# Optimization experiments

Measured on AMD Instinct MI355X. Metric: run time of the kernel, lower is better.

The kernel has to match this reference:

```python
import jax, jax.numpy as jnp
import numpy as np

S, B, D = 2048, 4, 1024

def setup_inputs() -> dict:
    key = jax.random.key(0)
    ks = jax.random.split(key, 7)
    std = 1.0 / np.sqrt(D)
    return {
        "x": jax.random.normal(ks[0], (S, B, D), dtype=jnp.float32),
        "Wq": jax.random.normal(ks[1], (D, D), dtype=jnp.float32) * std,
        "bq": jax.random.normal(ks[2], (D,), dtype=jnp.float32) * std,
        "Wk": jax.random.normal(ks[3], (D, D), dtype=jnp.float32) * std,
        "bk": jax.random.normal(ks[4], (D,), dtype=jnp.float32) * std,
        "Wv": jax.random.normal(ks[5], (D, D), dtype=jnp.float32) * std,
        "bv": jax.random.normal(ks[6], (D,), dtype=jnp.float32) * std,
    }

def reference(x, Wq, bq, Wk, bk, Wv, bv):
    # x: (S, B, D); flatten(start_dim=2) is a no-op for 3D input
    xf = jnp.transpose(x, (1, 0, 2))  # (B, S, D)
    # torch Linear: y = x @ W.T + b (W is (out, in))
    q = jnp.einsum('bsd,ed->bse', xf, Wq) + bq
    k = jnp.einsum('bsd,ed->bse', xf, Wk) + bk
    v = jnp.einsum('bsd,ed->bse', xf, Wv) + bv
    scale = 1.0 / jnp.sqrt(jnp.asarray(x.shape[-1], dtype=x.dtype))
    scores = jnp.einsum('bqd,bkd->bqk', q, k) * scale  # (B, S, S)
    attn = jax.nn.softmax(scores, axis=-1)
    weighted = jnp.einsum('bqk,bkd->bqd', attn, v)  # (B, S, D)
    # Faithful to torch.reshape(weighted, x.shape): reshape, NOT transpose back
    return jnp.reshape(weighted, x.shape)
```

## Files before the change

kernel.cpp:

```cpp
#include <hip/hip_runtime.h>
#include <math.h>

typedef float  f4   __attribute__((ext_vector_type(4)));
typedef float  f32x4 __attribute__((ext_vector_type(4)));
typedef short  bf16x8 __attribute__((ext_vector_type(8)));
typedef unsigned short u16x8 __attribute__((ext_vector_type(8)));

#define S_ 2048
#define B_ 4
#define D_ 1024

__device__ __forceinline__ unsigned short f2bf(float f) {
    unsigned u = __builtin_bit_cast(unsigned, f);
    u = (u + 0x7FFFu + ((u >> 16) & 1u)) >> 16;
    return (unsigned short)u;
}

#define GLOAD16(gsrc, ldst) \
    __builtin_amdgcn_global_load_lds((const __attribute__((address_space(1))) void*)(gsrc), \
                                     (__attribute__((address_space(3))) void*)(ldst), 16, 0, 0)


__global__ __launch_bounds__(128)
void convert_x(const float* __restrict__ x, unsigned short* __restrict__ xb)
{
    const int bid = blockIdx.x;
    const int b = bid & (B_ - 1);
    const int s = bid >> 2;
    const int t = threadIdx.x;
    const float* in = x + (size_t)bid * D_ + t * 8;
    unsigned short* out = xb + ((size_t)b * S_ + s) * D_ + t * 8;
    f4 lo = *(const f4*)in;
    f4 hi = *(const f4*)(in + 4);
    u16x8 o;
#pragma unroll
    for (int j = 0; j < 4; j++) { o[j] = f2bf(lo[j]); o[4 + j] = f2bf(hi[j]); }
    *(u16x8*)out = o;
}

__global__ __launch_bounds__(256)
void convert_w(const float* __restrict__ W0, const float* __restrict__ W1,
               const float* __restrict__ W2, unsigned short* __restrict__ dst)
{
    const float* src = (blockIdx.z == 0) ? W0 : (blockIdx.z == 1) ? W1 : W2;
    unsigned short* d = dst + (size_t)blockIdx.z * D_ * D_;
    size_t i = ((size_t)blockIdx.x * 256 + threadIdx.x) * 8;
    f4 lo = *(const f4*)(src + i);
    f4 hi = *(const f4*)(src + i + 4);
    u16x8 o;
#pragma unroll
    for (int j = 0; j < 4; j++) { o[j] = f2bf(lo[j]); o[4 + j] = f2bf(hi[j]); }
    *(u16x8*)(d + i) = o;
}

__global__ __launch_bounds__(256)
void transpose_v(const unsigned short* __restrict__ vb, unsigned short* __restrict__ vt)
{
    __shared__ unsigned short tile[64][66];
    const int t = threadIdx.x;
    const int s0 = blockIdx.x * 64, d0 = blockIdx.y * 64, b = blockIdx.z;
    const int rr = t >> 3, c8 = (t & 7) * 8;
#pragma unroll
    for (int p = 0; p < 2; p++) {
        int r = rr + p * 32;
        u16x8 v = *(const u16x8*)(vb + ((size_t)b * S_ + s0 + r) * D_ + d0 + c8);
#pragma unroll
        for (int j = 0; j < 8; j++) tile[r][c8 + j] = v[j];
    }
    __syncthreads();
#pragma unroll
    for (int p = 0; p < 2; p++) {
        int r = rr + p * 32;
        u16x8 o;
#pragma unroll
        for (int j = 0; j < 8; j++) o[j] = tile[c8 + j][r];
        *(u16x8*)(vt + ((size_t)b * D_ + d0 + r) * S_ + s0 + c8) = o;
    }
}

template<bool BIAS, bool OBF16>
__global__ __launch_bounds__(256)
void gemm_bt(const unsigned short* __restrict__ A, const unsigned short* __restrict__ B,
             const float* __restrict__ bias, void* __restrict__ C,
             int lda, int ldb, int ldc, int K, float alpha,
             size_t sA, size_t sB, size_t sC)
{
    __shared__ unsigned short sm[8192];

    const unsigned short* Ab = A + blockIdx.z * sA;
    const unsigned short* Bb = B + blockIdx.z * sB;

    const int t   = threadIdx.x;
    const int w   = t >> 6;
    const int ln  = t & 63;
    const int m0  = blockIdx.x * 128;
    const int n0  = blockIdx.y * 128;
    const int wm  = (w >> 1) * 64;
    const int wn  = (w & 1) * 64;
    const int c15 = ln & 15;
    const int k16 = ln >> 4;

    const char* srcA0 = (const char*)(Ab + (size_t)(m0 + 32 * w +      (ln >> 2)) * lda + (ln & 3) * 8);
    const char* srcA1 = (const char*)(Ab + (size_t)(m0 + 32 * w + 16 + (ln >> 2)) * lda + (ln & 3) * 8);
    const char* srcB0 = (const char*)(Bb + (size_t)(n0 + 32 * w +      (ln >> 2)) * ldb + (ln & 3) * 8);
    const char* srcB1 = (const char*)(Bb + (size_t)(n0 + 32 * w + 16 + (ln >> 2)) * ldb + (ln & 3) * 8);

    unsigned short* ldsA0 = &sm[(2 * w) * 512];
    unsigned short* ldsA1 = &sm[(2 * w + 1) * 512];
    unsigned short* ldsB0 = &sm[4096 + (2 * w) * 512];
    unsigned short* ldsB1 = &sm[4096 + (2 * w + 1) * 512];

    const int offA = (wm + c15) * 32 + k16 * 8;
    const int offB = 4096 + (wn + c15) * 32 + k16 * 8;

    f32x4 acc[4][4];
#pragma unroll
    for (int i = 0; i < 4; i++)
#pragma unroll
        for (int j = 0; j < 4; j++) acc[i][j] = (f32x4)0.f;

    for (int k0 = 0; k0 < K; k0 += 32) {
        size_t kb = (size_t)k0 * 2;
        GLOAD16(srcA0 + kb, ldsA0);
        GLOAD16(srcA1 + kb, ldsA1);
        GLOAD16(srcB0 + kb, ldsB0);
        GLOAD16(srcB1 + kb, ldsB1);
        __syncthreads();

        bf16x8 af[4], bf[4];
#pragma unroll
        for (int i = 0; i < 4; i++) af[i] = *(const bf16x8*)&sm[offA + i * 512];
#pragma unroll
        for (int j = 0; j < 4; j++) bf[j] = *(const bf16x8*)&sm[offB + j * 512];
#pragma unroll
        for (int i = 0; i < 4; i++)
#pragma unroll
            for (int j = 0; j < 4; j++)
                acc[i][j] = __builtin_amdgcn_mfma_f32_16x16x32_bf16(af[i], bf[j], acc[i][j], 0, 0, 0);
        __syncthreads();
    }

    float bv[4];
#pragma unroll
    for (int j = 0; j < 4; j++)
        bv[j] = BIAS ? bias[n0 + wn + j * 16 + c15] : 0.f;

#pragma unroll
    for (int i = 0; i < 4; i++) {
#pragma unroll
        for (int j = 0; j < 4; j++) {
            int col = n0 + wn + j * 16 + c15;
#pragma unroll
            for (int r = 0; r < 4; r++) {
                int row = m0 + wm + i * 16 + k16 * 4 + r;
                float vv = acc[i][j][r] * alpha + bv[j];
                if (OBF16)
                    ((unsigned short*)C + blockIdx.z * sC)[(size_t)row * ldc + col] = f2bf(vv);
                else
                    ((float*)C + blockIdx.z * sC)[(size_t)row * ldc + col] = vv;
            }
        }
    }
}

__global__ __launch_bounds__(256)
void softmax_rows(float* __restrict__ P)
{
    float* p = P + (size_t)blockIdx.x * S_;
    const int t = threadIdx.x;

    f4 v0 = *(f4*)&p[t * 8];
    f4 v1 = *(f4*)&p[t * 8 + 4];

    float mx = v0[0];
#pragma unroll
    for (int j = 0; j < 4; j++) { mx = fmaxf(mx, v0[j]); mx = fmaxf(mx, v1[j]); }
#pragma unroll
    for (int off = 32; off > 0; off >>= 1) mx = fmaxf(mx, __shfl_xor(mx, off));

    __shared__ float rmax[4], rsum[4];
    if ((t & 63) == 0) rmax[t >> 6] = mx;
    __syncthreads();
    mx = fmaxf(fmaxf(rmax[0], rmax[1]), fmaxf(rmax[2], rmax[3]));

    float sum = 0.f;
#pragma unroll
    for (int j = 0; j < 4; j++) {
        v0[j] = __expf(v0[j] - mx); sum += v0[j];
        v1[j] = __expf(v1[j] - mx); sum += v1[j];
    }
#pragma unroll
    for (int off = 32; off > 0; off >>= 1) sum += __shfl_xor(sum, off);
    if ((t & 63) == 0) rsum[t >> 6] = sum;
    __syncthreads();
    sum = rsum[0] + rsum[1] + rsum[2] + rsum[3];

    float inv = 1.f / sum;
    unsigned short* ob = (unsigned short*)p;
    u16x8 o;
#pragma unroll
    for (int j = 0; j < 4; j++) { o[j] = f2bf(v0[j] * inv); o[4 + j] = f2bf(v1[j] * inv); }
    __syncthreads();
    *(u16x8*)&ob[t * 8] = o;
}


extern "C" void kernel_launch(void* const* d_in, const int* in_sizes, int n_in,
                              void* d_out, int out_size, void* d_ws, size_t ws_size,
                              hipStream_t stream)
{
    const float* x  = (const float*)d_in[0];
    const float* Wq = (const float*)d_in[1];
    const float* bq = (const float*)d_in[2];
    const float* Wk = (const float*)d_in[3];
    const float* bk = (const float*)d_in[4];
    const float* Wv = (const float*)d_in[5];
    const float* bv = (const float*)d_in[6];
    float* out = (float*)d_out;

    const size_t nTok = (size_t)B_ * S_;
    const size_t nQKV = nTok * D_;
    char* ws = (char*)d_ws;

    unsigned short* xb = (unsigned short*)ws;                     ws += nQKV * 2;
    unsigned short* wb = (unsigned short*)ws;                     ws += 3 * D_ * D_ * 2;
    unsigned short* qb = (unsigned short*)ws;                     ws += nQKV * 2;
    unsigned short* kb = (unsigned short*)ws;                     ws += nQKV * 2;
    unsigned short* vb = (unsigned short*)ws;                     ws += nQKV * 2;
    unsigned short* vt = (unsigned short*)ws;                     ws += nQKV * 2;
    float*          sc = (float*)ws;                              ws += (size_t)B_ * S_ * S_ * 4;
    if ((size_t)(ws - (char*)d_ws) > ws_size) return;

    dim3 blk(256, 1, 1);

    convert_x<<<dim3(S_ * B_, 1, 1), dim3(128, 1, 1), 0, stream>>>(x, xb);
    convert_w<<<dim3(512, 1, 3), blk, 0, stream>>>(Wq, Wk, Wv, wb);

    dim3 g1(64, 8, 1);
    gemm_bt<true, true><<<g1, blk, 0, stream>>>(xb, wb,              bq, qb, D_, D_, D_, D_, 1.f, 0, 0, 0);
    gemm_bt<true, true><<<g1, blk, 0, stream>>>(xb, wb + D_ * D_,     bk, kb, D_, D_, D_, D_, 1.f, 0, 0, 0);
    gemm_bt<true, true><<<g1, blk, 0, stream>>>(xb, wb + 2 * D_ * D_, bv, vb, D_, D_, D_, D_, 1.f, 0, 0, 0);

    transpose_v<<<dim3(S_ / 64, D_ / 64, B_), blk, 0, stream>>>(vb, vt);

    dim3 g2(16, 16, B_);
    gemm_bt<false, false><<<g2, blk, 0, stream>>>(qb, kb, nullptr, sc, D_, D_, S_, D_, 0.03125f,
                                                  (size_t)S_ * D_, (size_t)S_ * D_, (size_t)S_ * S_);

    softmax_rows<<<dim3(B_ * S_, 1, 1), blk, 0, stream>>>(sc);

    dim3 g4(16, 8, B_);
    gemm_bt<false, false><<<g4, blk, 0, stream>>>((const unsigned short*)sc, vt, nullptr, out,
                                                  2 * S_, S_, D_, S_, 1.f,
                                                  (size_t)S_ * S_ * 2, (size_t)S_ * D_, (size_t)S_ * D_);
}
```

Baseline: 324.6 us.

## Replace GEMM with double-buffered swizzled 256x256 tiles and fuse QKV projection

Replaces the single-buffered 128x128 GEMM with a templated kernel. The new kernel uses 64-wide K steps, double-buffered LDS with prefetch interleaved between MFMA groups, XOR-swizzled LDS layout, workgroup rasterization swizzle, and setprio around MFMA. The three Q/K/V projections become one GEMM against concatenated weights and biases, writing an interleaved qkv buffer that later kernels read through strides. This is meant to cut kernel launches, improve data reuse and hide global load latency, at the cost of more registers and LDS per block, which may lower occupancy.

```diff
diff --git a/kernel.cpp b/kernel.cpp
--- a/kernel.cpp
+++ b/kernel.cpp
@@ -1,8 +1,8 @@
 #include <hip/hip_runtime.h>
 #include <math.h>
 
-typedef float  f4   __attribute__((ext_vector_type(4)));
-typedef float  f32x4 __attribute__((ext_vector_type(4)));
+typedef float  f4     __attribute__((ext_vector_type(4)));
+typedef float  f32x4  __attribute__((ext_vector_type(4)));
 typedef short  bf16x8 __attribute__((ext_vector_type(8)));
 typedef unsigned short u16x8 __attribute__((ext_vector_type(8)));
 
@@ -54,16 +54,25 @@
 }
 
 __global__ __launch_bounds__(256)
-void transpose_v(const unsigned short* __restrict__ vb, unsigned short* __restrict__ vt)
-{
-    __shared__ unsigned short tile[64][66];
+void convert_bias(const float* __restrict__ b0, const float* __restrict__ b1,
+                  const float* __restrict__ b2, float* __restrict__ bcat)
+{
+    int i = blockIdx.x * 256 + threadIdx.x;
+    int z = i >> 10, j = i & 1023;
+    bcat[i] = (z == 0) ? b0[j] : (z == 1) ? b1[j] : b2[j];
+}
+
+__global__ __launch_bounds__(256)
+void transpose_v(const unsigned short* __restrict__ qkv, unsigned short* __restrict__ vt)
+{
+    __shared__ unsigned short tile[64][72];
     const int t = threadIdx.x;
     const int s0 = blockIdx.x * 64, d0 = blockIdx.y * 64, b = blockIdx.z;
     const int rr = t >> 3, c8 = (t & 7) * 8;
 #pragma unroll
     for (int p = 0; p < 2; p++) {
         int r = rr + p * 32;
-        u16x8 v = *(const u16x8*)(vb + ((size_t)b * S_ + s0 + r) * D_ + d0 + c8);
+        u16x8 v = *(const u16x8*)(qkv + ((size_t)b * S_ + s0 + r) * 3072 + 2048 + d0 + c8);
 #pragma unroll
         for (int j = 0; j < 8; j++) tile[r][c8 + j] = v[j];
     }
@@ -78,86 +87,149 @@
     }
 }
 
-template<bool BIAS, bool OBF16>
-__global__ __launch_bounds__(256)
-void gemm_bt(const unsigned short* __restrict__ A, const unsigned short* __restrict__ B,
-             const float* __restrict__ bias, void* __restrict__ C,
-             int lda, int ldb, int ldc, int K, float alpha,
-             size_t sA, size_t sB, size_t sC)
-{
-    __shared__ unsigned short sm[8192];
+template<int BM, int BN, int WM, int WN, bool BIAS, bool OBF16>
+__global__ __launch_bounds__(WM*WN*64, 2)
+void gemm2(const unsigned short* __restrict__ A, const unsigned short* __restrict__ B,
+           const float* __restrict__ bias, void* __restrict__ C,
+           int lda, int ldb, int ldc, int K, float alpha,
+           size_t sA, size_t sB, size_t sC)
+{
+    constexpr int T   = WM * WN * 64;
+    constexpr int WTM = BM / WM, WTN = BN / WN;
+    constexpr int MR  = WTM / 16, NR = WTN / 16;
+    constexpr int MH  = MR / 2,  NH = NR / 2;
+    constexpr int ABYTES = BM * 128;
+    constexpr int BUFB   = (BM + BN) * 128;
+
+    __shared__ char sm[2 * BUFB] __attribute__((aligned(128)));
+
+    const int t  = threadIdx.x;
+    const int w  = t >> 6, ln = t & 63;
+    const int wr = w / WN, wc = w % WN;
+    const int c15 = ln & 15, k16 = ln >> 4;
+
+    const int gx  = gridDim.x;
+    const int nwg = gx * gridDim.y;
+    const int l0  = blockIdx.y * gx + blockIdx.x;
+    const int cpx = nwg >> 3;
+    const int lsw = (l0 & 7) * cpx + (l0 >> 3);
+    const int m0  = (lsw % gx) * BM;
+    const int n0  = (lsw / gx) * BN;
 
     const unsigned short* Ab = A + blockIdx.z * sA;
     const unsigned short* Bb = B + blockIdx.z * sB;
 
-    const int t   = threadIdx.x;
-    const int w   = t >> 6;
-    const int ln  = t & 63;
-    const int m0  = blockIdx.x * 128;
-    const int n0  = blockIdx.y * 128;
-    const int wm  = (w >> 1) * 64;
-    const int wn  = (w & 1) * 64;
-    const int c15 = ln & 15;
-    const int k16 = ln >> 4;
-
-    const char* srcA0 = (const char*)(Ab + (size_t)(m0 + 32 * w +      (ln >> 2)) * lda + (ln & 3) * 8);
-    const char* srcA1 = (const char*)(Ab + (size_t)(m0 + 32 * w + 16 + (ln >> 2)) * lda + (ln & 3) * 8);
-    const char* srcB0 = (const char*)(Bb + (size_t)(n0 + 32 * w +      (ln >> 2)) * ldb + (ln & 3) * 8);
-    const char* srcB1 = (const char*)(Bb + (size_t)(n0 + 32 * w + 16 + (ln >> 2)) * ldb + (ln & 3) * 8);
-
-    unsigned short* ldsA0 = &sm[(2 * w) * 512];
-    unsigned short* ldsA1 = &sm[(2 * w + 1) * 512];
-    unsigned short* ldsB0 = &sm[4096 + (2 * w) * 512];
-    unsigned short* ldsB1 = &sm[4096 + (2 * w + 1) * 512];
-
-    const int offA = (wm + c15) * 32 + k16 * 8;
-    const int offB = 4096 + (wn + c15) * 32 + k16 * 8;
-
-    f32x4 acc[4][4];
-#pragma unroll
-    for (int i = 0; i < 4; i++)
-#pragma unroll
-        for (int j = 0; j < 4; j++) acc[i][j] = (f32x4)0.f;
-
-    for (int k0 = 0; k0 < K; k0 += 32) {
-        size_t kb = (size_t)k0 * 2;
-        GLOAD16(srcA0 + kb, ldsA0);
-        GLOAD16(srcA1 + kb, ldsA1);
-        GLOAD16(srcB0 + kb, ldsB0);
-        GLOAD16(srcB1 + kb, ldsB1);
-        __syncthreads();
-
-        bf16x8 af[4], bf[4];
-#pragma unroll
-        for (int i = 0; i < 4; i++) af[i] = *(const bf16x8*)&sm[offA + i * 512];
-#pragma unroll
-        for (int j = 0; j < 4; j++) bf[j] = *(const bf16x8*)&sm[offB + j * 512];
-#pragma unroll
-        for (int i = 0; i < 4; i++)
-#pragma unroll
-            for (int j = 0; j < 4; j++)
-                acc[i][j] = __builtin_amdgcn_mfma_f32_16x16x32_bf16(af[i], bf[j], acc[i][j], 0, 0, 0);
-        __syncthreads();
-    }
-
-    float bv[4];
-#pragma unroll
-    for (int j = 0; j < 4; j++)
-        bv[j] = BIAS ? bias[n0 + wn + j * 16 + c15] : 0.f;
-
-#pragma unroll
-    for (int i = 0; i < 4; i++) {
-#pragma unroll
-        for (int j = 0; j < 4; j++) {
-            int col = n0 + wn + j * 16 + c15;
+    const char* srcp[8];
+    int ldso[8];
+#pragma unroll
+    for (int l = 0; l < 8; l++) {
+        int p = (l * T + t) * 16;
+        int q = p ^ (((p >> 9) & 3) << 5);
+        if (q < ABYTES) {
+            int r = q >> 7, cb = q & 127;
+            srcp[l] = (const char*)(Ab + (size_t)(m0 + r) * lda) + cb;
+        } else {
+            int q2 = q - ABYTES;
+            int r = q2 >> 7, cb = q2 & 127;
+            srcp[l] = (const char*)(Bb + (size_t)(n0 + r) * ldb) + cb;
+        }
+        ldso[l] = (l * T + (t & ~63)) * 16;
+    }
+
+    const int rbA   = (wr * WTM + c15) * 128 + k16 * 16;
+    const int xorA  = ((rbA >> 9) & 3) << 5;
+    const int bA0   = rbA ^ xorA;
+    const int bA1   = (rbA + 64) ^ xorA;
+    const int rbB   = (wc * WTN + c15) * 128 + k16 * 16;
+    const int xorB  = ((rbB >> 9) & 3) << 5;
+    const int bB0   = ABYTES + (rbB ^ xorB);
+    const int bB1   = ABYTES + ((rbB + 64) ^ xorB);
+
+    f32x4 acc[MR][NR];
+#pragma unroll
+    for (int i = 0; i < MR; i++)
+#pragma unroll
+        for (int j = 0; j < NR; j++) acc[i][j] = (f32x4)0.f;
+
+#pragma unroll
+    for (int l = 0; l < 8; l++) GLOAD16(srcp[l], sm + ldso[l]);
+
+    const int NT = K >> 6;
+    int cur = 0;
+    for (int kt = 0; kt < NT; ++kt) {
+        asm volatile("s_waitcnt vmcnt(0)" ::: "memory");
+        __builtin_amdgcn_s_barrier();
+        const char* rb  = sm + cur * BUFB;
+        char*       wbuf = sm + (cur ^ 1) * BUFB;
+        const size_t kbn = (size_t)(kt + 1) * 128;
+        const bool  st  = (kt + 1 < NT);
+
+        bf16x8 Bfr[2][NH][2];
+        int ph = 0;
+#pragma unroll
+        for (int mh = 0; mh < 2; mh++) {
+            bf16x8 Afr[MH][2];
+#pragma unroll
+            for (int i = 0; i < MH; i++) {
+                Afr[i][0] = *(const bf16x8*)(rb + bA0 + (mh * MH + i) * 2048);
+                Afr[i][1] = *(const bf16x8*)(rb + bA1 + (mh * MH + i) * 2048);
+            }
+#pragma unroll
+            for (int nh = 0; nh < 2; nh++) {
+                if (st && ph == 0) {
+                    GLOAD16(srcp[0] + kbn, wbuf + ldso[0]);
+                    GLOAD16(srcp[1] + kbn, wbuf + ldso[1]);
+                    GLOAD16(srcp[2] + kbn, wbuf + ldso[2]);
+                    GLOAD16(srcp[3] + kbn, wbuf + ldso[3]);
+                }
+                if (st && ph == 1) {
+                    GLOAD16(srcp[4] + kbn, wbuf + ldso[4]);
+                    GLOAD16(srcp[5] + kbn, wbuf + ldso[5]);
+                    GLOAD16(srcp[6] + kbn, wbuf + ldso[6]);
+                    GLOAD16(srcp[7] + kbn, wbuf + ldso[7]);
+                }
+                if (mh == 0) {
+#pragma unroll
+                    for (int j = 0; j < NH; j++) {
+                        Bfr[nh][j][0] = *(const bf16x8*)(rb + bB0 + (nh * NH + j) * 2048);
+                        Bfr[nh][j][1] = *(const bf16x8*)(rb + bB1 + (nh * NH + j) * 2048);
+                    }
+                }
+                __builtin_amdgcn_s_setprio(1);
+#pragma unroll
+                for (int i = 0; i < MH; i++)
+#pragma unroll
+                    for (int j = 0; j < NH; j++) {
+                        acc[mh*MH+i][nh*NH+j] = __builtin_amdgcn_mfma_f32_16x16x32_bf16(
+                            Afr[i][0], Bfr[nh][j][0], acc[mh*MH+i][nh*NH+j], 0, 0, 0);
+                        acc[mh*MH+i][nh*NH+j] = __builtin_amdgcn_mfma_f32_16x16x32_bf16(
+                            Afr[i][1], Bfr[nh][j][1], acc[mh*MH+i][nh*NH+j], 0, 0, 0);
+                    }
+                __builtin_amdgcn_s_setprio(0);
+                ph++;
+            }
+        }
+        cur ^= 1;
+    }
+
+    float bvv[NR];
+#pragma unroll
+    for (int j = 0; j < NR; j++)
+        bvv[j] = BIAS ? bias[n0 + wc * WTN + j * 16 + c15] : 0.f;
+
+#pragma unroll
+    for (int mi = 0; mi < MR; mi++) {
+        const int row = m0 + wr * WTM + mi * 16 + k16 * 4;
+#pragma unroll
+        for (int nj = 0; nj < NR; nj++) {
+            const int col = n0 + wc * WTN + nj * 16 + c15;
 #pragma unroll
             for (int r = 0; r < 4; r++) {
-                int row = m0 + wm + i * 16 + k16 * 4 + r;
-                float vv = acc[i][j][r] * alpha + bv[j];
+                float vv = acc[mi][nj][r] * alpha + bvv[nj];
                 if (OBF16)
-                    ((unsigned short*)C + blockIdx.z * sC)[(size_t)row * ldc + col] = f2bf(vv);
+                    ((unsigned short*)C + blockIdx.z * sC)[(size_t)(row + r) * ldc + col] = f2bf(vv);
                 else
-                    ((float*)C + blockIdx.z * sC)[(size_t)row * ldc + col] = vv;
+                    ((float*)C + blockIdx.z * sC)[(size_t)(row + r) * ldc + col] = vv;
             }
         }
     }
@@ -219,38 +291,32 @@
     float* out = (float*)d_out;
 
     const size_t nTok = (size_t)B_ * S_;
-    const size_t nQKV = nTok * D_;
     char* ws = (char*)d_ws;
 
-    unsigned short* xb = (unsigned short*)ws;                     ws += nQKV * 2;
-    unsigned short* wb = (unsigned short*)ws;                     ws += 3 * D_ * D_ * 2;
-    unsigned short* qb = (unsigned short*)ws;                     ws += nQKV * 2;
-    unsigned short* kb = (unsigned short*)ws;                     ws += nQKV * 2;
-    unsigned short* vb = (unsigned short*)ws;                     ws += nQKV * 2;
-    unsigned short* vt = (unsigned short*)ws;                     ws += nQKV * 2;
-    float*          sc = (float*)ws;                              ws += (size_t)B_ * S_ * S_ * 4;
+    unsigned short* xb   = (unsigned short*)ws;   ws += nTok * D_ * 2;
+    unsigned short* wcat = (unsigned short*)ws;   ws += (size_t)3 * D_ * D_ * 2;
+    float*          bcat = (float*)ws;            ws += 3 * D_ * 4;
+    unsigned short* qkv  = (unsigned short*)ws;   ws += nTok * 3 * D_ * 2;
+    unsigned short* vt   = (unsigned short*)ws;   ws += nTok * D_ * 2;
+    float*          sc   = (float*)ws;            ws += (size_t)B_ * S_ * S_ * 4;
     if ((size_t)(ws - (char*)d_ws) > ws_size) return;
 
-    dim3 blk(256, 1, 1);
-
-    convert_x<<<dim3(S_ * B_, 1, 1), dim3(128, 1, 1), 0, stream>>>(x, xb);
-    convert_w<<<dim3(512, 1, 3), blk, 0, stream>>>(Wq, Wk, Wv, wb);
-
-    dim3 g1(64, 8, 1);
-    gemm_bt<true, true><<<g1, blk, 0, stream>>>(xb, wb,              bq, qb, D_, D_, D_, D_, 1.f, 0, 0, 0);
-    gemm_bt<true, true><<<g1, blk, 0, stream>>>(xb, wb + D_ * D_,     bk, kb, D_, D_, D_, D_, 1.f, 0, 0, 0);
-    gemm_bt<true, true><<<g1, blk, 0, stream>>>(xb, wb + 2 * D_ * D_, bv, vb, D_, D_, D_, D_, 1.f, 0, 0, 0);
-
-    transpose_v<<<dim3(S_ / 64, D_ / 64, B_), blk, 0, stream>>>(vb, vt);
-
-    dim3 g2(16, 16, B_);
-    gemm_bt<false, false><<<g2, blk, 0, stream>>>(qb, kb, nullptr, sc, D_, D_, S_, D_, 0.03125f,
-                                                  (size_t)S_ * D_, (size_t)S_ * D_, (size_t)S_ * S_);
-
-    softmax_rows<<<dim3(B_ * S_, 1, 1), blk, 0, stream>>>(sc);
-
-    dim3 g4(16, 8, B_);
-    gemm_bt<false, false><<<g4, blk, 0, stream>>>((const unsigned short*)sc, vt, nullptr, out,
-                                                  2 * S_, S_, D_, S_, 1.f,
-                                                  (size_t)S_ * S_ * 2, (size_t)S_ * D_, (size_t)S_ * D_);
-}
+    convert_x<<<dim3(S_ * B_), dim3(128), 0, stream>>>(x, xb);
+    convert_w<<<dim3(512, 1, 3), dim3(256), 0, stream>>>(Wq, Wk, Wv, wcat);
+    convert_bias<<<dim3(12), dim3(256), 0, stream>>>(bq, bk, bv, bcat);
+
+    gemm2<256, 256, 2, 4, true, true><<<dim3(32, 12, 1), dim3(512), 0, stream>>>(
+        xb, wcat, bcat, qkv, D_, D_, 3 * D_, D_, 1.f, 0, 0, 0);
+
+    transpose_v<<<dim3(S_ / 64, D_ / 64, B_), dim3(256), 0, stream>>>(qkv, vt);
+
+    gemm2<256, 256, 2, 4, false, false><<<dim3(8, 8, B_), dim3(512), 0, stream>>>(
+        qkv, qkv + D_, nullptr, sc, 3 * D_, 3 * D_, S_, D_, 0.03125f,
+        (size_t)S_ * 3 * D_, (size_t)S_ * 3 * D_, (size_t)S_ * S_);
+
+    softmax_rows<<<dim3(B_ * S_), dim3(256), 0, stream>>>(sc);
+
+    gemm2<128, 128, 2, 2, false, false><<<dim3(16, 8, B_), dim3(256), 0, stream>>>(
+        (const unsigned short*)sc, vt, nullptr, out, 2 * S_, S_, D_, S_, 1.f,
+        (size_t)S_ * S_ * 2, (size_t)D_ * S_, (size_t)S_ * D_);
+}
```

New measurement: 267.4 us. 1.21x faster.
